# Optimization experiments

Measured on AMD Instinct MI355X. Metric: run time of the kernel, lower is better.

## Reference

```python
import jax, jax.numpy as jnp
import numpy as np

EPS = 1e-5
EMBED_DIM = 1024
CTX_DIM = 768
NUM_HEADS = 16
DH = EMBED_DIM // NUM_HEADS
# Faithful to torch source: embed_dim // num_heads ** 0.5 parses as embed_dim // (num_heads**0.5)
SCALE = EMBED_DIM // (NUM_HEADS ** 0.5)  # = 256.0


def ws_conv1x1(x, w, b, mask):
    # weight-standardized 1x1 conv1d: w [O, I, 1], x [B, I, T]
    w2 = w[..., 0]
    mu = jnp.mean(w2, axis=1, keepdims=True)
    var = jnp.var(w2, axis=1, keepdims=True)
    wn = (w2 - mu) * jax.lax.rsqrt(var + EPS)
    y = jnp.einsum('oi,bit->bot', wn, x) + b[None, :, None]
    if mask is not None:
        y = jnp.where(mask, y, 0.0)  # mask [B,1,T] bool
    return y


def layernorm(x, g, b):
    # normalize over last axis
    mu = jnp.mean(x, axis=-1, keepdims=True)
    var = jnp.var(x, axis=-1, keepdims=True)
    return (x - mu) * jax.lax.rsqrt(var + EPS) * g + b


def setup_inputs() -> dict:
    key = jax.random.key(0)
    ks = jax.random.split(key, 16)
    B, T, S = 4, 1024, 1024
    inp = {
        'x': jax.random.normal(ks[0], (B, EMBED_DIM, T), dtype=jnp.float32),
        'context': jax.random.normal(ks[1], (B, CTX_DIM, S), dtype=jnp.float32),
        'mask': jax.random.randint(ks[2], (B, 1, T), 0, 2).astype(bool),
        'mask_ctx': jax.random.randint(ks[3], (B, 1, S), 0, 2).astype(bool),
        'qw': jax.random.normal(ks[4], (EMBED_DIM, EMBED_DIM, 1), dtype=jnp.float32) * 0.02,
        'qb': jnp.zeros((EMBED_DIM,), jnp.float32),
        'kw': jax.random.normal(ks[5], (EMBED_DIM, CTX_DIM, 1), dtype=jnp.float32) * 0.02,
        'kb': jnp.zeros((EMBED_DIM,), jnp.float32),
        'vw': jax.random.normal(ks[6], (EMBED_DIM, CTX_DIM, 1), dtype=jnp.float32) * 0.02,
        'vb': jnp.zeros((EMBED_DIM,), jnp.float32),
        'ow': jax.random.normal(ks[7], (EMBED_DIM, EMBED_DIM, 1), dtype=jnp.float32) * 0.02,
        'ob': jnp.zeros((EMBED_DIM,), jnp.float32),
        'gq': jnp.ones((DH,), jnp.float32), 'bq': jnp.zeros((DH,), jnp.float32),
        'gk': jnp.ones((DH,), jnp.float32), 'bk': jnp.zeros((DH,), jnp.float32),
        'gv': jnp.ones((DH,), jnp.float32), 'bv': jnp.zeros((DH,), jnp.float32),
    }
    return inp


def reference(x, context, mask, mask_ctx, qw, qb, kw, kb, vw, vb, ow, ob, gq, bq, gk, bk, gv, bv):
    B, E, T = x.shape
    S = context.shape[-1]
    q = ws_conv1x1(x, qw, qb, mask)            # [B,E,T]
    k = ws_conv1x1(context, kw, kb, mask_ctx)  # [B,E,S]
    v = ws_conv1x1(context, vw, vb, mask_ctx)  # [B,E,S]
    # split heads -> [B,H,dh,L]
    q = q.reshape(B, NUM_HEADS, DH, T)
    k = k.reshape(B, NUM_HEADS, DH, S)
    v = v.reshape(B, NUM_HEADS, DH, S)
    # middle_norm: LayerNorm over dh (applied on transposed layout)
    q = jnp.swapaxes(layernorm(jnp.swapaxes(q, -1, -2), gq, bq), -1, -2)
    k = jnp.swapaxes(layernorm(jnp.swapaxes(k, -1, -2), gk, bk), -1, -2)
    v = jnp.swapaxes(layernorm(jnp.swapaxes(v, -1, -2), gv, bv), -1, -2)
    # scores: k^T @ q -> [B,H,S,T]
    scores = jnp.einsum('bhds,bhdt->bhst', k, q) / SCALE
    scores = jnp.where(mask[:, :, None, :], scores, -1e9)  # mask over query dim T
    scores = jax.nn.softmax(scores, axis=-1)               # softmax over T (as in source)
    scores = jnp.where(mask_ctx[:, :, :, None], scores, 0.0)
    out = jnp.einsum('bhds,bhst->bhdt', v, scores)          # v @ scores -> [B,H,dh,T]
    out = out.reshape(B, E, T)
    out = ws_conv1x1(out, ow, ob, mask) + x
    return out
```

## Files before the change

kernel.cpp:

```cpp
#include <hip/hip_runtime.h>

#define NB 4
#define TT 1024
#define SS 1024
#define EE 1024
#define CCH 768
#define NH 16
#define DHH 64
#define EPSF 1e-5f
#define QSCALE (1.4426950408889634f / 256.0f)

typedef unsigned short u16;
typedef __attribute__((ext_vector_type(8))) short short8;
typedef __attribute__((ext_vector_type(8))) unsigned short u16x8;
typedef __attribute__((ext_vector_type(4))) unsigned short u16x4;
typedef __attribute__((ext_vector_type(4))) float f32x4;

__device__ __forceinline__ u16 f2bu(float f) {
    union { float f; unsigned u; } x; x.f = f;
    unsigned r = x.u + 0x7fffu + ((x.u >> 16) & 1u);
    return (u16)(r >> 16);
}
__device__ __forceinline__ float bu2f(u16 u) {
    union { unsigned u; float f; } x; x.u = ((unsigned)u) << 16; return x.f;
}

#if __has_builtin(__builtin_amdgcn_exp2f)
#define EXP2(x) __builtin_amdgcn_exp2f(x)
#else
#define EXP2(x) exp2f(x)
#endif

#define MFMA16(a, b, c) __builtin_amdgcn_mfma_f32_16x16x32_bf16((a), (b), (c), 0, 0, 0)

__global__ __launch_bounds__(256) void ws_norm4(
    const float* __restrict__ qw, const float* __restrict__ kw,
    const float* __restrict__ vw, const float* __restrict__ ow,
    u16* __restrict__ wqn, u16* __restrict__ wkn,
    u16* __restrict__ wvn, u16* __restrict__ won) {
    int mat = blockIdx.y;
    const float* w = mat == 0 ? qw : (mat == 1 ? kw : (mat == 2 ? vw : ow));
    u16* wn = mat == 0 ? wqn : (mat == 1 ? wkn : (mat == 2 ? wvn : won));
    int I = (mat == 1 || mat == 2) ? CCH : EE;
    int row = blockIdx.x;
    const float* wr = w + (size_t)row * I;
    float s = 0.f, s2 = 0.f;
    for (int i = threadIdx.x; i < I; i += 256) { float v = wr[i]; s += v; s2 += v * v; }
#pragma unroll
    for (int off = 32; off > 0; off >>= 1) { s += __shfl_down(s, off); s2 += __shfl_down(s2, off); }
    __shared__ float sa[4], sb[4], smean, srstd;
    int wid = threadIdx.x >> 6;
    if ((threadIdx.x & 63) == 0) { sa[wid] = s; sb[wid] = s2; }
    __syncthreads();
    if (threadIdx.x == 0) {
        float ts = sa[0] + sa[1] + sa[2] + sa[3];
        float ts2 = sb[0] + sb[1] + sb[2] + sb[3];
        float mean = ts / (float)I;
        float var = ts2 / (float)I - mean * mean;
        smean = mean; srstd = rsqrtf(var + EPSF);
    }
    __syncthreads();
    float mean = smean, r = srstd;
    u16* wo = wn + (size_t)row * I;
    for (int i = threadIdx.x; i < I; i += 256) wo[i] = f2bu((wr[i] - mean) * r);
}

__global__ __launch_bounds__(256) void transpose2(
    const float* __restrict__ x, const float* __restrict__ ctx,
    u16* __restrict__ xT, u16* __restrict__ cT) {
    __shared__ float tile[64][65];
    int yy = blockIdx.y;
    int mat = yy < 16 ? 0 : 1;
    int r0 = (mat == 0 ? yy : yy - 16) * 64;
    int R = mat == 0 ? EE : CCH;
    const float* in = mat == 0 ? x : ctx;
    u16* out = mat == 0 ? xT : cT;
    int c0 = blockIdx.x * 64, b = blockIdx.z;
    const float* ip = in + (size_t)b * R * 1024;
    u16* op = out + (size_t)b * R * 1024;
    int tid = threadIdx.x;
#pragma unroll
    for (int m = 0; m < 16; m++) {
        int id = tid + 256 * m; int r = id >> 6, c = id & 63;
        tile[r][c] = ip[(size_t)(r0 + r) * 1024 + c0 + c];
    }
    __syncthreads();
#pragma unroll
    for (int m = 0; m < 16; m++) {
        int id = tid + 256 * m; int rr = id >> 6, cc = id & 63;
        op[(size_t)(c0 + rr) * R + r0 + cc] = tile[cc][rr];
    }
}
__global__ __launch_bounds__(256) void transpose2_f2b(
    const float* __restrict__ x, const float* __restrict__ ctx,
    u16* __restrict__ xT, u16* __restrict__ cT) {
    __shared__ float tile[64][65];
    int yy = blockIdx.y;
    int mat = yy < 16 ? 0 : 1;
    int r0 = (mat == 0 ? yy : yy - 16) * 64;
    int R = mat == 0 ? EE : CCH;
    const float* in = mat == 0 ? x : ctx;
    u16* out = mat == 0 ? xT : cT;
    int c0 = blockIdx.x * 64, b = blockIdx.z;
    const float* ip = in + (size_t)b * R * 1024;
    u16* op = out + (size_t)b * R * 1024;
    int tid = threadIdx.x;
#pragma unroll
    for (int m = 0; m < 16; m++) {
        int id = tid + 256 * m; int r = id >> 6, c = id & 63;
        tile[r][c] = ip[(size_t)(r0 + r) * 1024 + c0 + c];
    }
    __syncthreads();
#pragma unroll
    for (int m = 0; m < 16; m++) {
        int id = tid + 256 * m; int rr = id >> 6, cc = id & 63;
        op[(size_t)(c0 + rr) * R + r0 + cc] = f2bu(tile[cc][rr]);
    }
}

__device__ __forceinline__ void proj_core(
    const u16* __restrict__ A, const u16* __restrict__ BT,
    const float* __restrict__ bias, const int* __restrict__ mask,
    const float* __restrict__ resid, u16* __restrict__ outB, float* __restrict__ outF,
    int O, int I, int L, int o0, int l0, int b,
    u16 (*at)[72], u16 (*bt)[72]) {
    int tid = threadIdx.x;
    int w = tid >> 6, lane = tid & 63, quad = lane >> 4, l16 = lane & 15;
    int wm = w & 1, wn = w >> 1;
    const u16* Bp = BT + (size_t)b * L * I;

    f32x4 acc[4][2] = {};
    for (int k0 = 0; k0 < I; k0 += 64) {
        __syncthreads();
#pragma unroll
        for (int m = 0; m < 4; m++) {
            int id = tid + 256 * m; int r = id >> 3, c = (id & 7) * 8;
            *(u16x8*)&at[r][c] = *(const u16x8*)&A[(size_t)(o0 + r) * I + k0 + c];
        }
#pragma unroll
        for (int m = 0; m < 2; m++) {
            int id = tid + 256 * m; int r = id >> 3, c = (id & 7) * 8;
            *(u16x8*)&bt[r][c] = *(const u16x8*)&Bp[(size_t)(l0 + r) * I + k0 + c];
        }
        __syncthreads();
#pragma unroll
        for (int ks = 0; ks < 64; ks += 32) {
            short8 af[4], bf[2];
#pragma unroll
            for (int i = 0; i < 4; i++)
                af[i] = *(const short8*)&at[wm * 64 + i * 16 + l16][ks + quad * 8];
#pragma unroll
            for (int j = 0; j < 2; j++)
                bf[j] = *(const short8*)&bt[wn * 32 + j * 16 + l16][ks + quad * 8];
#pragma unroll
            for (int mt = 0; mt < 4; mt++)
#pragma unroll
                for (int nt = 0; nt < 2; nt++)
                    acc[mt][nt] = MFMA16(af[mt], bf[nt], acc[mt][nt]);
        }
    }
    const int* mrow = mask + (size_t)b * L;
#pragma unroll
    for (int nt = 0; nt < 2; nt++) {
        int l = l0 + wn * 32 + nt * 16 + l16;
        int mval = mrow[l];
#pragma unroll
        for (int mt = 0; mt < 4; mt++) {
#pragma unroll
            for (int reg = 0; reg < 4; reg++) {
                int o = o0 + wm * 64 + mt * 16 + quad * 4 + reg;
                float v = mval ? (acc[mt][nt][reg] + bias[o]) : 0.f;
                size_t off = ((size_t)b * O + o) * L + l;
                if (resid) v += resid[off];
                if (outF) outF[off] = v; else outB[off] = f2bu(v);
            }
        }
    }
}

__global__ __launch_bounds__(256) void proj_qkv(
    const u16* __restrict__ wq, const u16* __restrict__ wk, const u16* __restrict__ wv,
    const u16* __restrict__ xT, const u16* __restrict__ cT,
    const float* __restrict__ qb, const float* __restrict__ kb, const float* __restrict__ vbi,
    const int* __restrict__ mask_t, const int* __restrict__ mask_c,
    u16* __restrict__ yq, u16* __restrict__ yk, u16* __restrict__ yv) {
    __shared__ u16 at[128][72];
    __shared__ u16 bt[64][72];
    int mat = blockIdx.y >> 3;
    int o0 = (blockIdx.y & 7) * 128;
    int l0 = blockIdx.x * 64;
    const u16* A = mat == 0 ? wq : (mat == 1 ? wk : wv);
    const u16* BT = mat == 0 ? xT : cT;
    const float* bias = mat == 0 ? qb : (mat == 1 ? kb : vbi);
    const int* mask = mat == 0 ? mask_t : mask_c;
    u16* out = mat == 0 ? yq : (mat == 1 ? yk : yv);
    int I = mat == 0 ? EE : CCH;
    proj_core(A, BT, bias, mask, nullptr, out, nullptr, EE, I, 1024, o0, l0,
              blockIdx.z, at, bt);
}

__global__ __launch_bounds__(256) void proj_o(
    const u16* __restrict__ won, const u16* __restrict__ aT,
    const float* __restrict__ obi, const int* __restrict__ mask,
    const float* __restrict__ x, float* __restrict__ out) {
    __shared__ u16 at[128][72];
    __shared__ u16 bt[64][72];
    proj_core(won, aT, obi, mask, x, nullptr, out, EE, EE, TT,
              blockIdx.y * 128, blockIdx.x * 64, blockIdx.z, at, bt);
}

__global__ __launch_bounds__(256) void ln_qk(
    const u16* __restrict__ yq, const u16* __restrict__ yk,
    const float* __restrict__ gq, const float* __restrict__ bq,
    const float* __restrict__ gk, const float* __restrict__ bk,
    u16* __restrict__ qT, u16* __restrict__ kT) {
    int part = blockIdx.x >> 8;
    const u16* y = part == 0 ? yq : yk;
    const float* g = part == 0 ? gq : gk;
    const float* be = part == 0 ? bq : bk;
    u16* outT = part == 0 ? qT : kT;
    float scale = part == 0 ? QSCALE : 1.0f;
    int idx = (blockIdx.x & 255) * 256 + threadIdx.x;
    int l = idx & 1023; int bh = idx >> 10;
    size_t base = ((size_t)bh * 64) * 1024 + l;
    float v[DHH]; float s = 0.f;
#pragma unroll
    for (int d = 0; d < DHH; d++) { v[d] = bu2f(y[base + (size_t)d * 1024]); s += v[d]; }
    float mean = s * (1.f / DHH);
    float s2 = 0.f;
#pragma unroll
    for (int d = 0; d < DHH; d++) { float dv = v[d] - mean; s2 += dv * dv; }
    float r = rsqrtf(s2 * (1.f / DHH) + EPSF);
    u16* o = outT + ((size_t)bh * 1024 + l) * DHH;
#pragma unroll
    for (int d = 0; d < DHH; d++)
        o[d] = f2bu(((v[d] - mean) * r * g[d] + be[d]) * scale);
}

__global__ __launch_bounds__(256) void ln_v_scale(u16* __restrict__ y,
                                                  const float* __restrict__ g,
                                                  const float* __restrict__ be,
                                                  const int* __restrict__ mask_ctx,
                                                  const float* __restrict__ lrow, int L) {
    int idx = blockIdx.x * 256 + threadIdx.x;
    int l = idx % L; int bh = idx / L; int b = bh / NH;
    size_t base = ((size_t)bh * 64) * L + l;
    float v[DHH]; float s = 0.f;
#pragma unroll
    for (int d = 0; d < DHH; d++) { v[d] = bu2f(y[base + (size_t)d * L]); s += v[d]; }
    float mean = s * (1.f / DHH);
    float s2 = 0.f;
#pragma unroll
    for (int d = 0; d < DHH; d++) { float dv = v[d] - mean; s2 += dv * dv; }
    float r = rsqrtf(s2 * (1.f / DHH) + EPSF);
    float lv = lrow[(size_t)bh * L + l];
    float wsc = (mask_ctx[(size_t)b * L + l] != 0 && lv > 0.f) ? (1.f / lv) : 0.f;
#pragma unroll
    for (int d = 0; d < DHH; d++)
        y[base + (size_t)d * L] = f2bu(((v[d] - mean) * r * g[d] + be[d]) * wsc);
}

__global__ __launch_bounds__(256) void attn_stats_mfma(
    const u16* __restrict__ qT, const u16* __restrict__ kT,
    const int* __restrict__ mask, float* __restrict__ lrow) {
    __shared__ u16 kt[64][72];
    __shared__ u16 qt[64][72];
    __shared__ float lp[4][64];
    int tid = threadIdx.x;
    int w = tid >> 6, lane = tid & 63, quad = lane >> 4, l16 = lane & 15;
    int s0 = blockIdx.x * 64, h = blockIdx.y, b = blockIdx.z;
    int head = b * NH + h;
    const u16* kp = kT + (size_t)head * SS * DHH;
    const u16* qp = qT + (size_t)head * TT * DHH;
    const int* mk = mask + (size_t)b * TT;
#pragma unroll
    for (int m = 0; m < 2; m++) {
        int id = tid + 256 * m; int r = id >> 3, c = (id & 7) * 8;
        *(u16x8*)&kt[r][c] = *(const u16x8*)&kp[(size_t)(s0 + r) * DHH + c];
    }
    float rl[4][4] = {};
    for (int t0 = 0; t0 < TT; t0 += 64) {
        __syncthreads();
#pragma unroll
        for (int m = 0; m < 2; m++) {
            int id = tid + 256 * m; int r = id >> 3, c = (id & 7) * 8;
            *(u16x8*)&qt[r][c] = *(const u16x8*)&qp[(size_t)(t0 + r) * DHH + c];
        }
        __syncthreads();
        int mval = mk[t0 + w * 16 + l16];
        f32x4 acc[4] = {};
#pragma unroll
        for (int ks = 0; ks < 64; ks += 32) {
            short8 bf = *(const short8*)&qt[w * 16 + l16][ks + quad * 8];
#pragma unroll
            for (int mt = 0; mt < 4; mt++) {
                short8 af = *(const short8*)&kt[mt * 16 + l16][ks + quad * 8];
                acc[mt] = MFMA16(af, bf, acc[mt]);
            }
        }
        if (mval) {
#pragma unroll
            for (int mt = 0; mt < 4; mt++)
#pragma unroll
                for (int reg = 0; reg < 4; reg++)
                    rl[mt][reg] += EXP2(acc[mt][reg]);
        }
    }
#pragma unroll
    for (int mt = 0; mt < 4; mt++) {
#pragma unroll
        for (int reg = 0; reg < 4; reg++) {
            float v = rl[mt][reg];
            v += __shfl_xor(v, 1); v += __shfl_xor(v, 2);
            v += __shfl_xor(v, 4); v += __shfl_xor(v, 8);
            if (l16 == 0) lp[w][mt * 16 + quad * 4 + reg] = v;
        }
    }
    __syncthreads();
    if (tid < 64)
        lrow[(size_t)head * SS + s0 + tid] = lp[0][tid] + lp[1][tid] + lp[2][tid] + lp[3][tid];
}

__global__ __launch_bounds__(256) void attn_pv_mfma(
    const u16* __restrict__ qT, const u16* __restrict__ kT, const u16* __restrict__ vs,
    const int* __restrict__ mask, u16* __restrict__ aT) {
    __shared__ u16 qt[64][72];
    __shared__ u16 kt[64][72];
    __shared__ u16 vt[64][72];
    __shared__ u16 pt[64][72];
    int tid = threadIdx.x;
    int w = tid >> 6, lane = tid & 63, quad = lane >> 4, l16 = lane & 15;
    int t0 = blockIdx.x * 64, h = blockIdx.y, b = blockIdx.z;
    int head = b * NH + h;
    const u16* qp = qT + (size_t)head * TT * DHH;
    const u16* kp = kT + (size_t)head * SS * DHH;
    const u16* vp = vs + ((size_t)head * DHH) * SS;
#pragma unroll
    for (int m = 0; m < 2; m++) {
        int id = tid + 256 * m; int r = id >> 3, c = (id & 7) * 8;
        *(u16x8*)&qt[r][c] = *(const u16x8*)&qp[(size_t)(t0 + r) * DHH + c];
    }
    int mkv = mask[(size_t)b * TT + t0 + w * 16 + l16];

    f32x4 oacc[4] = {};
    for (int s0 = 0; s0 < SS; s0 += 64) {
        __syncthreads();
#pragma unroll
        for (int m = 0; m < 2; m++) {
            int id = tid + 256 * m; int r = id >> 3, c = (id & 7) * 8;
            *(u16x8*)&kt[r][c] = *(const u16x8*)&kp[(size_t)(s0 + r) * DHH + c];
            *(u16x8*)&vt[r][c] = *(const u16x8*)&vp[(size_t)r * SS + s0 + c];
        }
        __syncthreads();
        f32x4 acc[4] = {};
#pragma unroll
        for (int ks = 0; ks < 64; ks += 32) {
            short8 bf = *(const short8*)&qt[w * 16 + l16][ks + quad * 8];
#pragma unroll
            for (int mt = 0; mt < 4; mt++) {
                short8 af = *(const short8*)&kt[mt * 16 + l16][ks + quad * 8];
                acc[mt] = MFMA16(af, bf, acc[mt]);
            }
        }
#pragma unroll
        for (int mt = 0; mt < 4; mt++) {
#pragma unroll
            for (int reg = 0; reg < 4; reg++) {
                int sl = mt * 16 + quad * 4 + reg;
                float p = mkv ? EXP2(acc[mt][reg]) : 0.f;
                pt[w * 16 + l16][sl] = f2bu(p);
            }
        }
        __syncthreads();
#pragma unroll
        for (int ks = 0; ks < 64; ks += 32) {
            short8 bf = *(const short8*)&pt[w * 16 + l16][ks + quad * 8];
#pragma unroll
            for (int mt = 0; mt < 4; mt++) {
                short8 af = *(const short8*)&vt[mt * 16 + l16][ks + quad * 8];
                oacc[mt] = MFMA16(af, bf, oacc[mt]);
            }
        }
    }
    __syncthreads();
    int tl = w * 16 + l16;
#pragma unroll
    for (int mt = 0; mt < 4; mt++) {
        u16x4 pk;
#pragma unroll
        for (int reg = 0; reg < 4; reg++) pk[reg] = f2bu(oacc[mt][reg]);
        *(u16x4*)&pt[tl][mt * 16 + quad * 4] = pk;
    }
    __syncthreads();
#pragma unroll
    for (int i = 0; i < 2; i++) {
        int id = tid * 2 + i;
        int r = id >> 3, c = (id & 7) * 8;
        *(u16x8*)&aT[((size_t)b * TT + t0 + r) * EE + h * 64 + c] =
            *(const u16x8*)&pt[r][c];
    }
}

extern "C" void kernel_launch(void* const* d_in, const int* in_sizes, int n_in,
                              void* d_out, int out_size, void* d_ws, size_t ws_size,
                              hipStream_t stream) {
    const float* x        = (const float*)d_in[0];
    const float* ctx      = (const float*)d_in[1];
    const int*   mask     = (const int*)d_in[2];
    const int*   mask_ctx = (const int*)d_in[3];
    const float* qw  = (const float*)d_in[4];
    const float* qbi = (const float*)d_in[5];
    const float* kw  = (const float*)d_in[6];
    const float* kbi = (const float*)d_in[7];
    const float* vw  = (const float*)d_in[8];
    const float* vbi = (const float*)d_in[9];
    const float* ow  = (const float*)d_in[10];
    const float* obi = (const float*)d_in[11];
    const float* gq = (const float*)d_in[12];
    const float* bq = (const float*)d_in[13];
    const float* gk = (const float*)d_in[14];
    const float* bk = (const float*)d_in[15];
    const float* gv = (const float*)d_in[16];
    const float* bv = (const float*)d_in[17];

    u16* p = (u16*)d_ws;
    u16* wqn = p; p += (size_t)EE * EE;
    u16* wkn = p; p += (size_t)EE * CCH;
    u16* wvn = p; p += (size_t)EE * CCH;
    u16* won = p; p += (size_t)EE * EE;
    u16* xT  = p; p += (size_t)NB * TT * EE;
    u16* cT  = p; p += (size_t)NB * SS * CCH;
    u16* yq  = p; p += (size_t)NB * EE * TT;
    u16* yk  = p; p += (size_t)NB * EE * SS;
    u16* yv  = p; p += (size_t)NB * EE * SS;
    u16* qT  = p; p += (size_t)NB * NH * TT * DHH;
    u16* kT  = p; p += (size_t)NB * NH * SS * DHH;
    float* lrow = (float*)p;
    u16* aT = yq;

    ws_norm4<<<dim3(1024, 4), 256, 0, stream>>>(qw, kw, vw, ow, wqn, wkn, wvn, won);

    transpose2_f2b<<<dim3(16, 28, NB), 256, 0, stream>>>(x, ctx, xT, cT);

    proj_qkv<<<dim3(16, 24, NB), 256, 0, stream>>>(
        wqn, wkn, wvn, xT, cT, qbi, kbi, vbi, mask, mask_ctx, yq, yk, yv);

    ln_qk<<<512, 256, 0, stream>>>(yq, yk, gq, bq, gk, bk, qT, kT);

    attn_stats_mfma<<<dim3(SS / 64, NH, NB), 256, 0, stream>>>(qT, kT, mask, lrow);
    ln_v_scale<<<(NB * NH * SS) / 256, 256, 0, stream>>>(yv, gv, bv, mask_ctx, lrow, SS);

    attn_pv_mfma<<<dim3(TT / 64, NH, NB), 256, 0, stream>>>(qT, kT, yv, mask, aT);

    proj_o<<<dim3(16, 8, NB), 256, 0, stream>>>(won, aT, obi, mask, x, (float*)d_out);
}
```

Baseline: 275.3 us.

## Fuse LayerNorms into projection and stats epilogues, add register prefetch to GEMM loops

```diff
diff --git a/kernel.cpp b/kernel.cpp
--- a/kernel.cpp
+++ b/kernel.cpp
@@ -65,32 +65,6 @@
     for (int i = threadIdx.x; i < I; i += 256) wo[i] = f2bu((wr[i] - mean) * r);
 }
 
-__global__ __launch_bounds__(256) void transpose2(
-    const float* __restrict__ x, const float* __restrict__ ctx,
-    u16* __restrict__ xT, u16* __restrict__ cT) {
-    __shared__ float tile[64][65];
-    int yy = blockIdx.y;
-    int mat = yy < 16 ? 0 : 1;
-    int r0 = (mat == 0 ? yy : yy - 16) * 64;
-    int R = mat == 0 ? EE : CCH;
-    const float* in = mat == 0 ? x : ctx;
-    u16* out = mat == 0 ? xT : cT;
-    int c0 = blockIdx.x * 64, b = blockIdx.z;
-    const float* ip = in + (size_t)b * R * 1024;
-    u16* op = out + (size_t)b * R * 1024;
-    int tid = threadIdx.x;
-#pragma unroll
-    for (int m = 0; m < 16; m++) {
-        int id = tid + 256 * m; int r = id >> 6, c = id & 63;
-        tile[r][c] = ip[(size_t)(r0 + r) * 1024 + c0 + c];
-    }
-    __syncthreads();
-#pragma unroll
-    for (int m = 0; m < 16; m++) {
-        int id = tid + 256 * m; int rr = id >> 6, cc = id & 63;
-        op[(size_t)(c0 + rr) * R + r0 + cc] = tile[cc][rr];
-    }
-}
 __global__ __launch_bounds__(256) void transpose2_f2b(
     const float* __restrict__ x, const float* __restrict__ ctx,
     u16* __restrict__ xT, u16* __restrict__ cT) {
@@ -118,31 +92,49 @@
     }
 }
 
-__device__ __forceinline__ void proj_core(
-    const u16* __restrict__ A, const u16* __restrict__ BT,
-    const float* __restrict__ bias, const int* __restrict__ mask,
-    const float* __restrict__ resid, u16* __restrict__ outB, float* __restrict__ outF,
-    int O, int I, int L, int o0, int l0, int b,
-    u16 (*at)[72], u16 (*bt)[72]) {
+__device__ __forceinline__ void gemm_core(
+    const u16* __restrict__ A, const u16* __restrict__ Bp, int I,
+    int o0, int l0, u16 (*at)[72], u16 (*bt)[72], f32x4 (&acc)[4][2]) {
     int tid = threadIdx.x;
     int w = tid >> 6, lane = tid & 63, quad = lane >> 4, l16 = lane & 15;
     int wm = w & 1, wn = w >> 1;
-    const u16* Bp = BT + (size_t)b * L * I;
-
-    f32x4 acc[4][2] = {};
+    u16x8 ra[4], rb[2];
+#pragma unroll
+    for (int m = 0; m < 4; m++) {
+        int id = tid + 256 * m; int r = id >> 3, c = (id & 7) * 8;
+        ra[m] = *(const u16x8*)&A[(size_t)(o0 + r) * I + c];
+    }
+#pragma unroll
+    for (int m = 0; m < 2; m++) {
+        int id = tid + 256 * m; int r = id >> 3, c = (id & 7) * 8;
+        rb[m] = *(const u16x8*)&Bp[(size_t)(l0 + r) * I + c];
+    }
     for (int k0 = 0; k0 < I; k0 += 64) {
         __syncthreads();
 #pragma unroll
         for (int m = 0; m < 4; m++) {
             int id = tid + 256 * m; int r = id >> 3, c = (id & 7) * 8;
-            *(u16x8*)&at[r][c] = *(const u16x8*)&A[(size_t)(o0 + r) * I + k0 + c];
+            *(u16x8*)&at[r][c] = ra[m];
         }
 #pragma unroll
         for (int m = 0; m < 2; m++) {
             int id = tid + 256 * m; int r = id >> 3, c = (id & 7) * 8;
-            *(u16x8*)&bt[r][c] = *(const u16x8*)&Bp[(size_t)(l0 + r) * I + k0 + c];
-        }
-        __syncthreads();
+            *(u16x8*)&bt[r][c] = rb[m];
+        }
+        __syncthreads();
+        int k1 = k0 + 64;
+        if (k1 < I) {
+#pragma unroll
+            for (int m = 0; m < 4; m++) {
+                int id = tid + 256 * m; int r = id >> 3, c = (id & 7) * 8;
+                ra[m] = *(const u16x8*)&A[(size_t)(o0 + r) * I + k1 + c];
+            }
+#pragma unroll
+            for (int m = 0; m < 2; m++) {
+                int id = tid + 256 * m; int r = id >> 3, c = (id & 7) * 8;
+                rb[m] = *(const u16x8*)&Bp[(size_t)(l0 + r) * I + k1 + c];
+            }
+        }
 #pragma unroll
         for (int ks = 0; ks < 64; ks += 32) {
             short8 af[4], bf[2];
@@ -157,23 +149,6 @@
 #pragma unroll
                 for (int nt = 0; nt < 2; nt++)
                     acc[mt][nt] = MFMA16(af[mt], bf[nt], acc[mt][nt]);
-        }
-    }
-    const int* mrow = mask + (size_t)b * L;
-#pragma unroll
-    for (int nt = 0; nt < 2; nt++) {
-        int l = l0 + wn * 32 + nt * 16 + l16;
-        int mval = mrow[l];
-#pragma unroll
-        for (int mt = 0; mt < 4; mt++) {
-#pragma unroll
-            for (int reg = 0; reg < 4; reg++) {
-                int o = o0 + wm * 64 + mt * 16 + quad * 4 + reg;
-                float v = mval ? (acc[mt][nt][reg] + bias[o]) : 0.f;
-                size_t off = ((size_t)b * O + o) * L + l;
-                if (resid) v += resid[off];
-                if (outF) outF[off] = v; else outB[off] = f2bu(v);
-            }
         }
     }
 }
@@ -183,20 +158,86 @@
     const u16* __restrict__ xT, const u16* __restrict__ cT,
     const float* __restrict__ qb, const float* __restrict__ kb, const float* __restrict__ vbi,
     const int* __restrict__ mask_t, const int* __restrict__ mask_c,
-    u16* __restrict__ yq, u16* __restrict__ yk, u16* __restrict__ yv) {
+    const float* __restrict__ gq, const float* __restrict__ bq,
+    const float* __restrict__ gk, const float* __restrict__ bk,
+    u16* __restrict__ qT, u16* __restrict__ kT, u16* __restrict__ yv) {
     __shared__ u16 at[128][72];
     __shared__ u16 bt[64][72];
+    __shared__ float sg[64], sbe[64], sbias[128];
+    int tid = threadIdx.x;
+    int w = tid >> 6, lane = tid & 63, quad = lane >> 4, l16 = lane & 15;
+    int wm = w & 1, wn = w >> 1;
     int mat = blockIdx.y >> 3;
     int o0 = (blockIdx.y & 7) * 128;
     int l0 = blockIdx.x * 64;
+    int b = blockIdx.z;
     const u16* A = mat == 0 ? wq : (mat == 1 ? wk : wv);
     const u16* BT = mat == 0 ? xT : cT;
     const float* bias = mat == 0 ? qb : (mat == 1 ? kb : vbi);
-    const int* mask = mat == 0 ? mask_t : mask_c;
-    u16* out = mat == 0 ? yq : (mat == 1 ? yk : yv);
+    const int* maskp = mat == 0 ? mask_t : mask_c;
     int I = mat == 0 ? EE : CCH;
-    proj_core(A, BT, bias, mask, nullptr, out, nullptr, EE, I, 1024, o0, l0,
-              blockIdx.z, at, bt);
+    if (mat < 2 && tid < 64) {
+        sg[tid] = (mat == 0 ? gq : gk)[tid];
+        sbe[tid] = (mat == 0 ? bq : bk)[tid];
+    }
+    if (tid < 128) sbias[tid] = bias[o0 + tid];
+
+    f32x4 acc[4][2] = {};
+    gemm_core(A, BT + (size_t)b * 1024 * I, I, o0, l0, at, bt, acc);
+
+    const int* mrow = maskp + (size_t)b * 1024;
+    if (mat < 2) {
+        u16* outT = mat == 0 ? qT : kT;
+        float scale = mat == 0 ? QSCALE : 1.0f;
+        int h = (o0 >> 6) + wm;
+        int bh = b * NH + h;
+#pragma unroll
+        for (int nt = 0; nt < 2; nt++) {
+            int l = l0 + wn * 32 + nt * 16 + l16;
+            int mval = mrow[l];
+            float vbuf[16];
+            float s = 0.f;
+#pragma unroll
+            for (int mt = 0; mt < 4; mt++)
+#pragma unroll
+                for (int reg = 0; reg < 4; reg++) {
+                    float v = mval ? (acc[mt][nt][reg] + sbias[wm * 64 + mt * 16 + quad * 4 + reg]) : 0.f;
+                    vbuf[mt * 4 + reg] = v; s += v;
+                }
+            s += __shfl_xor(s, 16); s += __shfl_xor(s, 32);
+            float mean = s * (1.f / 64);
+            float s2 = 0.f;
+#pragma unroll
+            for (int i = 0; i < 16; i++) { float dv = vbuf[i] - mean; s2 += dv * dv; }
+            s2 += __shfl_xor(s2, 16); s2 += __shfl_xor(s2, 32);
+            float r = rsqrtf(s2 * (1.f / 64) + EPSF);
+            u16* op = outT + ((size_t)bh * 1024 + l) * 64;
+#pragma unroll
+            for (int mt = 0; mt < 4; mt++) {
+                u16x4 pk;
+#pragma unroll
+                for (int reg = 0; reg < 4; reg++) {
+                    int d = mt * 16 + quad * 4 + reg;
+                    pk[reg] = f2bu(((vbuf[mt * 4 + reg] - mean) * r * sg[d] + sbe[d]) * scale);
+                }
+                *(u16x4*)&op[mt * 16 + quad * 4] = pk;
+            }
+        }
+    } else {
+#pragma unroll
+        for (int nt = 0; nt < 2; nt++) {
+            int l = l0 + wn * 32 + nt * 16 + l16;
+            int mval = mrow[l];
+#pragma unroll
+            for (int mt = 0; mt < 4; mt++)
+#pragma unroll
+                for (int reg = 0; reg < 4; reg++) {
+                    int o = o0 + wm * 64 + mt * 16 + quad * 4 + reg;
+                    float v = mval ? (acc[mt][nt][reg] + sbias[wm * 64 + mt * 16 + quad * 4 + reg]) : 0.f;
+                    yv[((size_t)b * EE + o) * 1024 + l] = f2bu(v);
+                }
+        }
+    }
 }
 
 __global__ __launch_bounds__(256) void proj_o(
@@ -205,64 +246,36 @@
     const float* __restrict__ x, float* __restrict__ out) {
     __shared__ u16 at[128][72];
     __shared__ u16 bt[64][72];
-    proj_core(won, aT, obi, mask, x, nullptr, out, EE, EE, TT,
-              blockIdx.y * 128, blockIdx.x * 64, blockIdx.z, at, bt);
-}
-
-__global__ __launch_bounds__(256) void ln_qk(
-    const u16* __restrict__ yq, const u16* __restrict__ yk,
-    const float* __restrict__ gq, const float* __restrict__ bq,
-    const float* __restrict__ gk, const float* __restrict__ bk,
-    u16* __restrict__ qT, u16* __restrict__ kT) {
-    int part = blockIdx.x >> 8;
-    const u16* y = part == 0 ? yq : yk;
-    const float* g = part == 0 ? gq : gk;
-    const float* be = part == 0 ? bq : bk;
-    u16* outT = part == 0 ? qT : kT;
-    float scale = part == 0 ? QSCALE : 1.0f;
-    int idx = (blockIdx.x & 255) * 256 + threadIdx.x;
-    int l = idx & 1023; int bh = idx >> 10;
-    size_t base = ((size_t)bh * 64) * 1024 + l;
-    float v[DHH]; float s = 0.f;
-#pragma unroll
-    for (int d = 0; d < DHH; d++) { v[d] = bu2f(y[base + (size_t)d * 1024]); s += v[d]; }
-    float mean = s * (1.f / DHH);
-    float s2 = 0.f;
-#pragma unroll
-    for (int d = 0; d < DHH; d++) { float dv = v[d] - mean; s2 += dv * dv; }
-    float r = rsqrtf(s2 * (1.f / DHH) + EPSF);
-    u16* o = outT + ((size_t)bh * 1024 + l) * DHH;
-#pragma unroll
-    for (int d = 0; d < DHH; d++)
-        o[d] = f2bu(((v[d] - mean) * r * g[d] + be[d]) * scale);
-}
-
-__global__ __launch_bounds__(256) void ln_v_scale(u16* __restrict__ y,
-                                                  const float* __restrict__ g,
-                                                  const float* __restrict__ be,
-                                                  const int* __restrict__ mask_ctx,
-                                                  const float* __restrict__ lrow, int L) {
-    int idx = blockIdx.x * 256 + threadIdx.x;
-    int l = idx % L; int bh = idx / L; int b = bh / NH;
-    size_t base = ((size_t)bh * 64) * L + l;
-    float v[DHH]; float s = 0.f;
-#pragma unroll
-    for (int d = 0; d < DHH; d++) { v[d] = bu2f(y[base + (size_t)d * L]); s += v[d]; }
-    float mean = s * (1.f / DHH);
-    float s2 = 0.f;
-#pragma unroll
-    for (int d = 0; d < DHH; d++) { float dv = v[d] - mean; s2 += dv * dv; }
-    float r = rsqrtf(s2 * (1.f / DHH) + EPSF);
-    float lv = lrow[(size_t)bh * L + l];
-    float wsc = (mask_ctx[(size_t)b * L + l] != 0 && lv > 0.f) ? (1.f / lv) : 0.f;
-#pragma unroll
-    for (int d = 0; d < DHH; d++)
-        y[base + (size_t)d * L] = f2bu(((v[d] - mean) * r * g[d] + be[d]) * wsc);
+    __shared__ float sbias[128];
+    int tid = threadIdx.x;
+    int w = tid >> 6, lane = tid & 63, quad = lane >> 4, l16 = lane & 15;
+    int wm = w & 1, wn = w >> 1;
+    int o0 = blockIdx.y * 128, l0 = blockIdx.x * 64, b = blockIdx.z;
+    if (tid < 128) sbias[tid] = obi[o0 + tid];
+    f32x4 acc[4][2] = {};
+    gemm_core(won, aT + (size_t)b * TT * EE, EE, o0, l0, at, bt, acc);
+    const int* mrow = mask + (size_t)b * TT;
+#pragma unroll
+    for (int nt = 0; nt < 2; nt++) {
+        int l = l0 + wn * 32 + nt * 16 + l16;
+        int mval = mrow[l];
+#pragma unroll
+        for (int mt = 0; mt < 4; mt++)
+#pragma unroll
+            for (int reg = 0; reg < 4; reg++) {
+                int o = o0 + wm * 64 + mt * 16 + quad * 4 + reg;
+                float v = mval ? (acc[mt][nt][reg] + sbias[wm * 64 + mt * 16 + quad * 4 + reg]) : 0.f;
+                size_t off = ((size_t)b * EE + o) * TT + l;
+                out[off] = v + x[off];
+            }
+    }
 }
 
 __global__ __launch_bounds__(256) void attn_stats_mfma(
     const u16* __restrict__ qT, const u16* __restrict__ kT,
-    const int* __restrict__ mask, float* __restrict__ lrow) {
+    const int* __restrict__ mask, const int* __restrict__ mask_ctx,
+    const float* __restrict__ gv, const float* __restrict__ bv,
+    u16* __restrict__ yv) {
     __shared__ u16 kt[64][72];
     __shared__ u16 qt[64][72];
     __shared__ float lp[4][64];
@@ -278,15 +291,29 @@
         int id = tid + 256 * m; int r = id >> 3, c = (id & 7) * 8;
         *(u16x8*)&kt[r][c] = *(const u16x8*)&kp[(size_t)(s0 + r) * DHH + c];
     }
+    u16x8 rq[2];
+#pragma unroll
+    for (int m = 0; m < 2; m++) {
+        int id = tid + 256 * m; int r = id >> 3, c = (id & 7) * 8;
+        rq[m] = *(const u16x8*)&qp[(size_t)r * DHH + c];
+    }
     float rl[4][4] = {};
     for (int t0 = 0; t0 < TT; t0 += 64) {
         __syncthreads();
 #pragma unroll
         for (int m = 0; m < 2; m++) {
             int id = tid + 256 * m; int r = id >> 3, c = (id & 7) * 8;
-            *(u16x8*)&qt[r][c] = *(const u16x8*)&qp[(size_t)(t0 + r) * DHH + c];
-        }
-        __syncthreads();
+            *(u16x8*)&qt[r][c] = rq[m];
+        }
+        __syncthreads();
+        int t1 = t0 + 64;
+        if (t1 < TT) {
+#pragma unroll
+            for (int m = 0; m < 2; m++) {
+                int id = tid + 256 * m; int r = id >> 3, c = (id & 7) * 8;
+                rq[m] = *(const u16x8*)&qp[(size_t)(t1 + r) * DHH + c];
+            }
+        }
         int mval = mk[t0 + w * 16 + l16];
         f32x4 acc[4] = {};
 #pragma unroll
@@ -317,8 +344,27 @@
         }
     }
     __syncthreads();
-    if (tid < 64)
-        lrow[(size_t)head * SS + s0 + tid] = lp[0][tid] + lp[1][tid] + lp[2][tid] + lp[3][tid];
+    if (tid < 64) {
+        int s = s0 + tid;
+        float lv = lp[0][tid] + lp[1][tid] + lp[2][tid] + lp[3][tid];
+        int mc = mask_ctx[(size_t)b * SS + s];
+        float wsc = (mc != 0 && lv > 0.f) ? (1.f / lv) : 0.f;
+        u16* vcol = yv + ((size_t)b * EE + h * 64) * SS + s;
+        float sm = 0.f, s2 = 0.f;
+#pragma unroll
+        for (int d = 0; d < DHH; d++) {
+            float v = bu2f(vcol[(size_t)d * SS]);
+            sm += v; s2 += v * v;
+        }
+        float mean = sm * (1.f / DHH);
+        float var = s2 * (1.f / DHH) - mean * mean;
+        float r = rsqrtf(var + EPSF);
+#pragma unroll
+        for (int d = 0; d < DHH; d++) {
+            float v = bu2f(vcol[(size_t)d * SS]);
+            vcol[(size_t)d * SS] = f2bu(((v - mean) * r * gv[d] + bv[d]) * wsc);
+        }
+    }
 }
 
 __global__ __launch_bounds__(256) void attn_pv_mfma(
@@ -340,7 +386,15 @@
         int id = tid + 256 * m; int r = id >> 3, c = (id & 7) * 8;
         *(u16x8*)&qt[r][c] = *(const u16x8*)&qp[(size_t)(t0 + r) * DHH + c];
     }
+    u16x8 rk[2], rv[2];
+#pragma unroll
+    for (int m = 0; m < 2; m++) {
+        int id = tid + 256 * m; int r = id >> 3, c = (id & 7) * 8;
+        rk[m] = *(const u16x8*)&kp[(size_t)r * DHH + c];
+        rv[m] = *(const u16x8*)&vp[(size_t)r * SS + c];
+    }
     int mkv = mask[(size_t)b * TT + t0 + w * 16 + l16];
+    int tl = w * 16 + l16;
 
     f32x4 oacc[4] = {};
     for (int s0 = 0; s0 < SS; s0 += 64) {
@@ -348,14 +402,23 @@
 #pragma unroll
         for (int m = 0; m < 2; m++) {
             int id = tid + 256 * m; int r = id >> 3, c = (id & 7) * 8;
-            *(u16x8*)&kt[r][c] = *(const u16x8*)&kp[(size_t)(s0 + r) * DHH + c];
-            *(u16x8*)&vt[r][c] = *(const u16x8*)&vp[(size_t)r * SS + s0 + c];
-        }
-        __syncthreads();
+            *(u16x8*)&kt[r][c] = rk[m];
+            *(u16x8*)&vt[r][c] = rv[m];
+        }
+        __syncthreads();
+        int s1 = s0 + 64;
+        if (s1 < SS) {
+#pragma unroll
+            for (int m = 0; m < 2; m++) {
+                int id = tid + 256 * m; int r = id >> 3, c = (id & 7) * 8;
+                rk[m] = *(const u16x8*)&kp[(size_t)(s1 + r) * DHH + c];
+                rv[m] = *(const u16x8*)&vp[(size_t)r * SS + s1 + c];
+            }
+        }
         f32x4 acc[4] = {};
 #pragma unroll
         for (int ks = 0; ks < 64; ks += 32) {
-            short8 bf = *(const short8*)&qt[w * 16 + l16][ks + quad * 8];
+            short8 bf = *(const short8*)&qt[tl][ks + quad * 8];
 #pragma unroll
             for (int mt = 0; mt < 4; mt++) {
                 short8 af = *(const short8*)&kt[mt * 16 + l16][ks + quad * 8];
@@ -364,17 +427,16 @@
         }
 #pragma unroll
         for (int mt = 0; mt < 4; mt++) {
-#pragma unroll
-            for (int reg = 0; reg < 4; reg++) {
-                int sl = mt * 16 + quad * 4 + reg;
-                float p = mkv ? EXP2(acc[mt][reg]) : 0.f;
-                pt[w * 16 + l16][sl] = f2bu(p);
-            }
+            u16x4 pk;
+#pragma unroll
+            for (int reg = 0; reg < 4; reg++)
+                pk[reg] = mkv ? f2bu(EXP2(acc[mt][reg])) : (u16)0;
+            *(u16x4*)&pt[tl][mt * 16 + quad * 4] = pk;
         }
         __syncthreads();
 #pragma unroll
         for (int ks = 0; ks < 64; ks += 32) {
-            short8 bf = *(const short8*)&pt[w * 16 + l16][ks + quad * 8];
+            short8 bf = *(const short8*)&pt[tl][ks + quad * 8];
 #pragma unroll
             for (int mt = 0; mt < 4; mt++) {
                 short8 af = *(const short8*)&vt[mt * 16 + l16][ks + quad * 8];
@@ -383,7 +445,6 @@
         }
     }
     __syncthreads();
-    int tl = w * 16 + l16;
 #pragma unroll
     for (int mt = 0; mt < 4; mt++) {
         u16x4 pk;
@@ -430,25 +491,21 @@
     u16* won = p; p += (size_t)EE * EE;
     u16* xT  = p; p += (size_t)NB * TT * EE;
     u16* cT  = p; p += (size_t)NB * SS * CCH;
-    u16* yq  = p; p += (size_t)NB * EE * TT;
-    u16* yk  = p; p += (size_t)NB * EE * SS;
     u16* yv  = p; p += (size_t)NB * EE * SS;
     u16* qT  = p; p += (size_t)NB * NH * TT * DHH;
     u16* kT  = p; p += (size_t)NB * NH * SS * DHH;
-    float* lrow = (float*)p;
-    u16* aT = yq;
+    u16* aT  = p; p += (size_t)NB * TT * EE;
 
     ws_norm4<<<dim3(1024, 4), 256, 0, stream>>>(qw, kw, vw, ow, wqn, wkn, wvn, won);
 
     transpose2_f2b<<<dim3(16, 28, NB), 256, 0, stream>>>(x, ctx, xT, cT);
 
     proj_qkv<<<dim3(16, 24, NB), 256, 0, stream>>>(
-        wqn, wkn, wvn, xT, cT, qbi, kbi, vbi, mask, mask_ctx, yq, yk, yv);
-
-    ln_qk<<<512, 256, 0, stream>>>(yq, yk, gq, bq, gk, bk, qT, kT);
-
-    attn_stats_mfma<<<dim3(SS / 64, NH, NB), 256, 0, stream>>>(qT, kT, mask, lrow);
-    ln_v_scale<<<(NB * NH * SS) / 256, 256, 0, stream>>>(yv, gv, bv, mask_ctx, lrow, SS);
+        wqn, wkn, wvn, xT, cT, qbi, kbi, vbi, mask, mask_ctx,
+        gq, bq, gk, bk, qT, kT, yv);
+
+    attn_stats_mfma<<<dim3(SS / 64, NH, NB), 256, 0, stream>>>(
+        qT, kT, mask, mask_ctx, gv, bv, yv);
 
     attn_pv_mfma<<<dim3(TT / 64, NH, NB), 256, 0, stream>>>(qT, kT, yv, mask, aT);
 
```

Result: faster. 252.0 us (-8.5%).
